# Performance work log

Measured on AMD Instinct MI355X. Metric: run time of the kernel, lower is better.

## Reference

```python
import jax, jax.numpy as jnp
import numpy as np

B, T, I, H, O = 128, 1024, 1, 512, 1


def setup_inputs() -> dict:
    key = jax.random.key(0)
    k = jax.random.split(key, 6)
    s = 1.0 / np.sqrt(H).astype(np.float32)
    x = jax.random.normal(k[0], (B, T, I), dtype=jnp.float32)
    Wx = jax.random.uniform(k[1], (I, 4 * H), jnp.float32, -s, s)   # input->gates
    Wh = jax.random.uniform(k[2], (H, 4 * H), jnp.float32, -s, s)   # hidden->gates
    b = jax.random.uniform(k[3], (4 * H,), jnp.float32, -s, s)      # gate bias
    Wl = jax.random.uniform(k[4], (H, O), jnp.float32, -s, s)       # readout
    bl = jax.random.uniform(k[5], (O,), jnp.float32, -s, s)
    return {"x": x, "Wx": Wx, "Wh": Wh, "b": b, "Wl": Wl, "bl": bl, "future": 0}


def reference(x, Wx, Wh, b, Wl, bl, future):
    # x: (B, T, I). Custom LSTM cell unrolled over time via lax.scan, with a
    # per-timestep linear readout (as in the original per-step loop).
    H_ = Wh.shape[0]
    h0 = jnp.zeros((x.shape[0], H_), dtype=x.dtype)
    c0 = jnp.zeros((x.shape[0], H_), dtype=x.dtype)

    def step(carry, xt):  # xt: (B, I)
        h, c = carry
        gates = xt @ Wx + h @ Wh + b            # (B, 4H)
        i, f, g, o = jnp.split(gates, 4, axis=-1)
        i = jax.nn.sigmoid(i)
        f = jax.nn.sigmoid(f)
        g = jnp.tanh(g)
        o = jax.nn.sigmoid(o)
        c = f * c + i * g
        h = o * jnp.tanh(c)
        y = h @ Wl + bl                          # (B, O)
        return (h, c), y

    (_, _), ys = jax.lax.scan(step, (h0, c0), jnp.swapaxes(x, 0, 1))
    # ys: (T, B, O) -> (B, T, O), matching torch.stack(outputs,1).squeeze(2)
    return jnp.swapaxes(ys, 0, 1)
```

## Files before the change

kernel.cpp:

```cpp
#include <hip/hip_runtime.h>
#include <hip/hip_fp16.h>


typedef _Float16 f16;
typedef _Float16 f16x8 __attribute__((ext_vector_type(8)));
typedef float f32x4 __attribute__((ext_vector_type(4)));

#define BATCH 128
#define TT 1024
#define HID 512

#define WPACK_OFF   0
#define WPACK_BYTES (16*4*2*16*64*16)
#define HBUF_OFF    WPACK_BYTES
#define HBUF_ELEMS  (BATCH*HID)
#define WL16_OFF    (HBUF_OFF + 4*HBUF_ELEMS*2)
#define HHIST_OFF   (WL16_OFF + 4096)
#define HHIST_BYTES ((size_t)TT * BATCH * HID * 2)
#define WS_NEEDED   ((size_t)HHIST_OFF + HHIST_BYTES)

__global__ __launch_bounds__(256) void init_kernel(const float* Wl, f16* wl16,
                                                   unsigned* hbuf) {
    int idx = blockIdx.x * 256 + threadIdx.x;
    hbuf[idx] = ((idx >> 15) == 0) ? 0u : 0x00010001u;
    if (idx < HID) wl16[idx] = (f16)Wl[idx];
}

__global__ __launch_bounds__(256) void pack_kernel(const float* __restrict__ Wh,
                                                   f16* __restrict__ wpack) {
    int tid  = blockIdx.x * 256 + threadIdx.x;
    int lane = tid & 63;
    int s    = (tid >> 6) & 15;
    int T    = (tid >> 10) & 1;
    int wv   = (tid >> 11) & 3;
    int cg   = tid >> 13;
    int l_lo = lane & 15, l_hi = lane >> 4;
    int jt = ((wv * 4) + s) & 15;
    int jj = l_lo >> 2, q = l_lo & 3;
    int c = q * 512 + cg * 32 + T * 16 + wv * 4 + jj;
    int kbase = jt * 32 + l_hi * 8;
    f16x8 v;
#pragma unroll
    for (int e = 0; e < 8; ++e) v[e] = (f16)Wh[(kbase + e) * 2048 + c];
    ((f16x8*)wpack)[tid] = v;
}

__device__ __forceinline__ float dot8(f16x8 a, f16x8 b, float acc) {
#if __has_builtin(__builtin_amdgcn_fdot2)
    acc = __builtin_amdgcn_fdot2(__builtin_shufflevector(a, a, 0, 1),
                                 __builtin_shufflevector(b, b, 0, 1), acc, false);
    acc = __builtin_amdgcn_fdot2(__builtin_shufflevector(a, a, 2, 3),
                                 __builtin_shufflevector(b, b, 2, 3), acc, false);
    acc = __builtin_amdgcn_fdot2(__builtin_shufflevector(a, a, 4, 5),
                                 __builtin_shufflevector(b, b, 4, 5), acc, false);
    acc = __builtin_amdgcn_fdot2(__builtin_shufflevector(a, a, 6, 7),
                                 __builtin_shufflevector(b, b, 6, 7), acc, false);
#else
#pragma unroll
    for (int e = 0; e < 8; ++e) acc += (float)a[e] * (float)b[e];
#endif
    return acc;
}

template<int CTRL>
__device__ __forceinline__ float dpp_qp(float v) {
    int r = __builtin_amdgcn_update_dpp(0, __builtin_bit_cast(int, v),
                                        CTRL, 0xF, 0xF, true);
    return __builtin_bit_cast(float, r);
}

__device__ __forceinline__ void quad_transpose(const f32x4& m, int p4,
                                               float& f0, float& f1,
                                               float& f2, float& f3) {
    float t0, e0, e1, e2, e3;
    t0 = dpp_qp<0xB1>(m[1]); e0 = (p4 & 1) ? t0 : m[0];
    t0 = dpp_qp<0xB1>(m[0]); e1 = (p4 & 1) ? m[1] : t0;
    t0 = dpp_qp<0xB1>(m[3]); e2 = (p4 & 1) ? t0 : m[2];
    t0 = dpp_qp<0xB1>(m[2]); e3 = (p4 & 1) ? m[3] : t0;
    t0 = dpp_qp<0x4E>(e2); f0 = (p4 & 2) ? t0 : e0;
    t0 = dpp_qp<0x4E>(e3); f1 = (p4 & 2) ? t0 : e1;
    t0 = dpp_qp<0x4E>(e0); f2 = (p4 & 2) ? e2 : t0;
    t0 = dpp_qp<0x4E>(e1); f3 = (p4 & 2) ? e3 : t0;
}

template<int MODE>
__global__ __launch_bounds__(256, 1) void lstm_kernel(
    const float* __restrict__ x, const float* __restrict__ Wx,
    const float* __restrict__ bvec, const float* __restrict__ blp,
    const f16* __restrict__ wpack, f16* __restrict__ hbuf,
    const f16* __restrict__ wl16, f16* __restrict__ hhist,
    float* __restrict__ out)
{
    const int tid = threadIdx.x;
    const int cg = blockIdx.x >> 3;
    const int bg = blockIdx.x & 7;
    const int w = tid >> 6, lane = tid & 63;
    const int l_lo = lane & 15, l_hi = lane >> 4;

    __shared__ f16 hsh[2][8192];
    __shared__ f16 wlsh[512];

    if (tid < 64)
        *(f16x8*)(wlsh + tid * 8) = *(const f16x8*)(wl16 + tid * 8);

    f16x8 bf0[16], bf1[16];
    {
        const f16x8* wp0 = (const f16x8*)wpack
                         + (size_t)(((cg * 4 + w) * 2 + 0) * 16) * 64 + lane;
        const f16x8* wp1 = (const f16x8*)wpack
                         + (size_t)(((cg * 4 + w) * 2 + 1) * 16) * 64 + lane;
#pragma unroll
        for (int s = 0; s < 16; ++s) { bf0[s] = wp0[s * 64]; bf1[s] = wp1[s * 64]; }
    }

    const int row  = l_hi * 4 + (l_lo & 3);
    const int u0 = cg * 32 + w * 4 + (l_lo >> 2);
    const int u1 = u0 + 16;
    const int bglob = bg * 16 + row;
    const float bi0 = bvec[0*512+u0], bfo0 = bvec[1*512+u0];
    const float bg0 = bvec[2*512+u0], bo0 = bvec[3*512+u0];
    const float bi1 = bvec[0*512+u1], bfo1 = bvec[1*512+u1];
    const float bg1 = bvec[2*512+u1], bo1 = bvec[3*512+u1];
    const float wxi0 = Wx[0*512+u0], wxf0 = Wx[1*512+u0];
    const float wxg0 = Wx[2*512+u0], wxo0 = Wx[3*512+u0];
    const float wxi1 = Wx[0*512+u1], wxf1 = Wx[1*512+u1];
    const float wxg1 = Wx[2*512+u1], wxo1 = Wx[3*512+u1];
    const float blv = blp[0];

    const int rd_base = bg * 8192 + ((w * 16 + l_hi) * 16 + l_lo) * 8;
    const int st_idx0 = bg * 8192 + ((u0 >> 3) * 16 + row) * 8 + (u0 & 7);
    const int st_idx1 = bg * 8192 + ((u1 >> 3) * 16 + row) * 8 + (u1 & 7);
    const int hist0 = (bg * 16 + row) * 512 + u0;
    const int hist1 = (bg * 16 + row) * 512 + u1;

    const int p4 = l_lo & 3;
    const int sx = (l_lo & 7) << 4;
    const int lbase = l_lo * 1024;
    const int base_ws = w * 256 + l_hi * 16;
    const int xrow = bglob * TT;

    float cst0 = 0.f, cst1 = 0.f;
    const int TLAST = (MODE == 0) ? (TT - 1) : TT;

    for (int t = 0; t <= TLAST; ++t) {
        const f16* hp = hbuf + (size_t)(t & 3) * HBUF_ELEMS + rd_base;
        const unsigned ep = (unsigned)((t >> 2) & 1) * 0x00010001u;
        float xv = x[xrow + (t < TT ? t : 0)];

        f16x8 s0, s1, s2, s3;
        for (;;) {
            asm volatile(
                "global_load_dwordx4 %0, %4, off sc0 sc1\n\t"
                "global_load_dwordx4 %1, %5, off sc0 sc1\n\t"
                "global_load_dwordx4 %2, %6, off sc0 sc1\n\t"
                "global_load_dwordx4 %3, %7, off sc0 sc1\n\t"
                "s_waitcnt vmcnt(0)"
                : "=&v"(s0), "=&v"(s1), "=&v"(s2), "=&v"(s3)
                : "v"(hp), "v"(hp + 512), "v"(hp + 1024), "v"(hp + 1536)
                : "memory");
            union { f16x8 v; unsigned u[4]; } b0, b1, b2, b3;
            b0.v = s0; b1.v = s1; b2.v = s2; b3.v = s3;
            unsigned bad =
                (((b0.u[0]^ep)|(b0.u[1]^ep)|(b0.u[2]^ep)|(b0.u[3]^ep)) |
                 ((b1.u[0]^ep)|(b1.u[1]^ep)|(b1.u[2]^ep)|(b1.u[3]^ep)) |
                 ((b2.u[0]^ep)|(b2.u[1]^ep)|(b2.u[2]^ep)|(b2.u[3]^ep)) |
                 ((b3.u[0]^ep)|(b3.u[1]^ep)|(b3.u[2]^ep)|(b3.u[3]^ep))) & 0x00010001u;
            if (__all(bad == 0u)) break;
        }
        __builtin_amdgcn_sched_barrier(0);

        char* hb = (char*)hsh[t & 1];
        const int wb = lbase + base_ws;
        *(f16x8*)(hb + ((wb +   0) ^ sx)) = s0;
        *(f16x8*)(hb + ((wb +  64) ^ sx)) = s1;
        *(f16x8*)(hb + ((wb + 128) ^ sx)) = s2;
        *(f16x8*)(hb + ((wb + 192) ^ sx)) = s3;

        f32x4 cA0 = {0,0,0,0}, cA1 = {0,0,0,0};
        if (t < TT) {
            cA0 = __builtin_amdgcn_mfma_f32_16x16x32_f16(s0, bf0[0], cA0, 0,0,0);
            cA1 = __builtin_amdgcn_mfma_f32_16x16x32_f16(s0, bf1[0], cA1, 0,0,0);
            cA0 = __builtin_amdgcn_mfma_f32_16x16x32_f16(s1, bf0[1], cA0, 0,0,0);
            cA1 = __builtin_amdgcn_mfma_f32_16x16x32_f16(s1, bf1[1], cA1, 0,0,0);
            cA0 = __builtin_amdgcn_mfma_f32_16x16x32_f16(s2, bf0[2], cA0, 0,0,0);
            cA1 = __builtin_amdgcn_mfma_f32_16x16x32_f16(s2, bf1[2], cA1, 0,0,0);
            cA0 = __builtin_amdgcn_mfma_f32_16x16x32_f16(s3, bf0[3], cA0, 0,0,0);
            cA1 = __builtin_amdgcn_mfma_f32_16x16x32_f16(s3, bf1[3], cA1, 0,0,0);
        }
        __syncthreads();

        if (t < TT) {
            f32x4 cB0 = {0,0,0,0}, cB1 = {0,0,0,0};
            f32x4 cC0 = {0,0,0,0}, cC1 = {0,0,0,0};
            f32x4 cD0 = {0,0,0,0}, cD1 = {0,0,0,0};
#pragma unroll
            for (int i = 0; i < 4; ++i) {
                f16x8 a1 = *(const f16x8*)(hb + ((lbase + ((base_ws + (4+i)*64) & 1023)) ^ sx));
                f16x8 a2 = *(const f16x8*)(hb + ((lbase + ((base_ws + (8+i)*64) & 1023)) ^ sx));
                f16x8 a3 = *(const f16x8*)(hb + ((lbase + ((base_ws + (12+i)*64) & 1023)) ^ sx));
                cB0 = __builtin_amdgcn_mfma_f32_16x16x32_f16(a1, bf0[ 4+i], cB0, 0,0,0);
                cB1 = __builtin_amdgcn_mfma_f32_16x16x32_f16(a1, bf1[ 4+i], cB1, 0,0,0);
                cC0 = __builtin_amdgcn_mfma_f32_16x16x32_f16(a2, bf0[ 8+i], cC0, 0,0,0);
                cC1 = __builtin_amdgcn_mfma_f32_16x16x32_f16(a2, bf1[ 8+i], cC1, 0,0,0);
                cD0 = __builtin_amdgcn_mfma_f32_16x16x32_f16(a3, bf0[12+i], cD0, 0,0,0);
                cD1 = __builtin_amdgcn_mfma_f32_16x16x32_f16(a3, bf1[12+i], cD1, 0,0,0);
            }
            f32x4 m0 = (cA0 + cB0) + (cC0 + cD0);
            f32x4 m1 = (cA1 + cB1) + (cC1 + cD1);

            float gi0, gf0, gg0, go0, gi1, gf1, gg1, go1;
            quad_transpose(m0, p4, gi0, gf0, gg0, go0);
            quad_transpose(m1, p4, gi1, gf1, gg1, go1);

            gi0 += xv * wxi0 + bi0;  gf0 += xv * wxf0 + bfo0;
            gg0 += xv * wxg0 + bg0;  go0 += xv * wxo0 + bo0;
            gi1 += xv * wxi1 + bi1;  gf1 += xv * wxf1 + bfo1;
            gg1 += xv * wxg1 + bg1;  go1 += xv * wxo1 + bo1;

            float iv0 = 1.f / (1.f + __expf(-gi0));
            float fv0 = 1.f / (1.f + __expf(-gf0));
            float gv0 = 2.f / (1.f + __expf(-2.f * gg0)) - 1.f;
            float ov0 = 1.f / (1.f + __expf(-go0));
            float iv1 = 1.f / (1.f + __expf(-gi1));
            float fv1 = 1.f / (1.f + __expf(-gf1));
            float gv1 = 2.f / (1.f + __expf(-2.f * gg1)) - 1.f;
            float ov1 = 1.f / (1.f + __expf(-go1));
            cst0 = fv0 * cst0 + iv0 * gv0;
            cst1 = fv1 * cst1 + iv1 * gv1;
            float hv0 = ov0 * (2.f / (1.f + __expf(-2.f * cst0)) - 1.f);
            float hv1 = ov1 * (2.f / (1.f + __expf(-2.f * cst1)) - 1.f);

            unsigned h0, h1;
            { union { f16 f; unsigned short s; } cv;
              cv.f = (f16)hv0; h0 = cv.s; cv.f = (f16)hv1; h1 = cv.s; }

            if ((MODE == 0) ? (t < TT - 1) : true) {
                const unsigned wtag = (unsigned)(((t + 1) >> 2) & 1);
                unsigned tg0 = (h0 & 0xFFFEu) | wtag;
                unsigned tg1 = (h1 & 0xFFFEu) | wtag;
                f16* dstb = hbuf + (size_t)((t + 1) & 3) * HBUF_ELEMS;
                asm volatile("global_store_short %0, %1, off sc0 sc1"
                             :: "v"(dstb + st_idx0), "v"(tg0) : "memory");
                asm volatile("global_store_short %0, %1, off sc0 sc1"
                             :: "v"(dstb + st_idx1), "v"(tg1) : "memory");
            }

            if (MODE == 0) {
                f16* hd = hhist + (size_t)t * (BATCH * HID);
                asm volatile("global_store_short %0, %1, off"
                             :: "v"(hd + hist0), "v"(h0) : "memory");
                asm volatile("global_store_short %0, %1, off"
                             :: "v"(hd + hist1), "v"(h1) : "memory");
            }
        }

        if (MODE == 1 && t >= 1 && cg == ((t >> 2) & 15) && w == (t & 3)) {
            float r0 = 0.f, r1 = 0.f, r2 = 0.f, r3 = 0.f;
#define WL(s) (*(const f16x8*)(wlsh + (((base_ws + (s)*64) & 1023) >> 1)))
            r0 = dot8(s0, WL(0), r0);
            r1 = dot8(s1, WL(1), r1);
            r2 = dot8(s2, WL(2), r2);
            r3 = dot8(s3, WL(3), r3);
#pragma unroll
            for (int i = 0; i < 4; ++i) {
                f16x8 a1 = *(const f16x8*)(hb + ((lbase + ((base_ws + (4+i)*64) & 1023)) ^ sx));
                f16x8 a2 = *(const f16x8*)(hb + ((lbase + ((base_ws + (8+i)*64) & 1023)) ^ sx));
                f16x8 a3 = *(const f16x8*)(hb + ((lbase + ((base_ws + (12+i)*64) & 1023)) ^ sx));
                r0 = dot8(a1, WL(4+i),  r0);
                r1 = dot8(a2, WL(8+i),  r1);
                r2 = dot8(a3, WL(12+i), r2);
            }
#undef WL
            float ry = (r0 + r1) + (r2 + r3);
            ry += __shfl_xor(ry, 16);
            ry += __shfl_xor(ry, 32);
            if (lane < 16)
                out[(bg * 16 + l_lo) * TT + (t - 1)] = blv + ry;
        }
    }
}

__global__ __launch_bounds__(256) void readout_kernel(
    const f16* __restrict__ hhist, const float* __restrict__ Wl,
    const float* __restrict__ blp, float* __restrict__ out)
{
    int gw = (blockIdx.x * 256 + threadIdx.x) >> 6;
    int lane = threadIdx.x & 63;
    int b = gw >> 7;
    int t0 = (gw & 127) * 8;
    const float4* wp = (const float4*)(Wl + lane * 8);
    float4 wa = wp[0], wb = wp[1];
    float blv = blp[0];
    const f16* hp = hhist + (size_t)t0 * (BATCH * HID) + b * HID + lane * 8;
#pragma unroll
    for (int j = 0; j < 8; ++j) {
        f16x8 h8 = *(const f16x8*)(hp + (size_t)j * (BATCH * HID));
        float p = (float)h8[0]*wa.x + (float)h8[1]*wa.y + (float)h8[2]*wa.z +
                  (float)h8[3]*wa.w + (float)h8[4]*wb.x + (float)h8[5]*wb.y +
                  (float)h8[6]*wb.z + (float)h8[7]*wb.w;
        p += __shfl_xor(p, 1);  p += __shfl_xor(p, 2);  p += __shfl_xor(p, 4);
        p += __shfl_xor(p, 8);  p += __shfl_xor(p, 16); p += __shfl_xor(p, 32);
        if (lane == 0) out[b * TT + t0 + j] = p + blv;
    }
}

extern "C" void kernel_launch(void* const* d_in, const int* in_sizes, int n_in,
                              void* d_out, int out_size, void* d_ws, size_t ws_size,
                              hipStream_t stream) {
    const float* x  = (const float*)d_in[0];
    const float* Wx = (const float*)d_in[1];
    const float* Wh = (const float*)d_in[2];
    const float* bv = (const float*)d_in[3];
    const float* Wl = (const float*)d_in[4];
    const float* bl = (const float*)d_in[5];
    float* out = (float*)d_out;
    char* ws = (char*)d_ws;

    f16* wpack = (f16*)(ws + WPACK_OFF);
    f16* hbuf  = (f16*)(ws + HBUF_OFF);
    f16* wl16  = (f16*)(ws + WL16_OFF);
    f16* hhist = (f16*)(ws + HHIST_OFF);

    init_kernel<<<512, 256, 0, stream>>>(Wl, wl16, (unsigned*)hbuf);
    pack_kernel<<<512, 256, 0, stream>>>(Wh, wpack);
    if (ws_size >= WS_NEEDED) {
        lstm_kernel<0><<<128, 256, 0, stream>>>(x, Wx, bv, bl, wpack, hbuf,
                                                wl16, hhist, out);
        readout_kernel<<<4096, 256, 0, stream>>>(hhist, Wl, bl, out);
    } else {
        lstm_kernel<1><<<128, 256, 0, stream>>>(x, Wx, bv, bl, wpack, hbuf,
                                                wl16, hhist, out);
    }
}
```

Baseline: 1.850 ms.

## Add shadow hidden-state buffer polled with sc0-only loads, periodic sc1 fallback

Each step's hidden state is now written to a second shadow buffer with device-scope (sc0) stores in addition to the system-coherent (sc0 sc1) buffer. The spin-wait poll reads the shadow copy with cheaper sc0 loads and falls back to the fully coherent buffer every eighth retry. The goal is to cut the latency of the inter-block exchange on the serial recurrence critical path. The cost is twice the store traffic per step, plus a risk of stale reads if sc0 loads do not observe cross-XCD writes, which the periodic sc1 fallback and tag check are meant to cover.

```diff
diff --git a/kernel.cpp b/kernel.cpp
--- a/kernel.cpp
+++ b/kernel.cpp
@@ -14,15 +14,18 @@
 #define WPACK_BYTES (16*4*2*16*64*16)
 #define HBUF_OFF    WPACK_BYTES
 #define HBUF_ELEMS  (BATCH*HID)
-#define WL16_OFF    (HBUF_OFF + 4*HBUF_ELEMS*2)
+#define SHBUF_OFF   (HBUF_OFF + 4*HBUF_ELEMS*2)
+#define WL16_OFF    (SHBUF_OFF + 4*HBUF_ELEMS*2)
 #define HHIST_OFF   (WL16_OFF + 4096)
 #define HHIST_BYTES ((size_t)TT * BATCH * HID * 2)
 #define WS_NEEDED   ((size_t)HHIST_OFF + HHIST_BYTES)
 
 __global__ __launch_bounds__(256) void init_kernel(const float* Wl, f16* wl16,
-                                                   unsigned* hbuf) {
+                                                   unsigned* hbuf, unsigned* hsh) {
     int idx = blockIdx.x * 256 + threadIdx.x;
-    hbuf[idx] = ((idx >> 15) == 0) ? 0u : 0x00010001u;
+    unsigned v = ((idx >> 15) == 0) ? 0u : 0x00010001u;
+    hbuf[idx] = v;
+    hsh[idx]  = v;
     if (idx < HID) wl16[idx] = (f16)Wl[idx];
 }
 
@@ -88,8 +91,8 @@
     const float* __restrict__ x, const float* __restrict__ Wx,
     const float* __restrict__ bvec, const float* __restrict__ blp,
     const f16* __restrict__ wpack, f16* __restrict__ hbuf,
-    const f16* __restrict__ wl16, f16* __restrict__ hhist,
-    float* __restrict__ out)
+    f16* __restrict__ hshadow, const f16* __restrict__ wl16,
+    f16* __restrict__ hhist, float* __restrict__ out)
 {
     const int tid = threadIdx.x;
     const int cg = blockIdx.x >> 3;
@@ -143,21 +146,35 @@
     const int TLAST = (MODE == 0) ? (TT - 1) : TT;
 
     for (int t = 0; t <= TLAST; ++t) {
-        const f16* hp = hbuf + (size_t)(t & 3) * HBUF_ELEMS + rd_base;
+        const f16* hp  = hbuf    + (size_t)(t & 3) * HBUF_ELEMS + rd_base;
+        const f16* hpS = hshadow + (size_t)(t & 3) * HBUF_ELEMS + rd_base;
         const unsigned ep = (unsigned)((t >> 2) & 1) * 0x00010001u;
         float xv = x[xrow + (t < TT ? t : 0)];
 
         f16x8 s0, s1, s2, s3;
+        unsigned r = 0;
         for (;;) {
-            asm volatile(
-                "global_load_dwordx4 %0, %4, off sc0 sc1\n\t"
-                "global_load_dwordx4 %1, %5, off sc0 sc1\n\t"
-                "global_load_dwordx4 %2, %6, off sc0 sc1\n\t"
-                "global_load_dwordx4 %3, %7, off sc0 sc1\n\t"
-                "s_waitcnt vmcnt(0)"
-                : "=&v"(s0), "=&v"(s1), "=&v"(s2), "=&v"(s3)
-                : "v"(hp), "v"(hp + 512), "v"(hp + 1024), "v"(hp + 1536)
-                : "memory");
+            if ((r++ & 7) != 7) {
+                asm volatile(
+                    "global_load_dwordx4 %0, %4, off sc0\n\t"
+                    "global_load_dwordx4 %1, %5, off sc0\n\t"
+                    "global_load_dwordx4 %2, %6, off sc0\n\t"
+                    "global_load_dwordx4 %3, %7, off sc0\n\t"
+                    "s_waitcnt vmcnt(0)"
+                    : "=&v"(s0), "=&v"(s1), "=&v"(s2), "=&v"(s3)
+                    : "v"(hpS), "v"(hpS + 512), "v"(hpS + 1024), "v"(hpS + 1536)
+                    : "memory");
+            } else {
+                asm volatile(
+                    "global_load_dwordx4 %0, %4, off sc0 sc1\n\t"
+                    "global_load_dwordx4 %1, %5, off sc0 sc1\n\t"
+                    "global_load_dwordx4 %2, %6, off sc0 sc1\n\t"
+                    "global_load_dwordx4 %3, %7, off sc0 sc1\n\t"
+                    "s_waitcnt vmcnt(0)"
+                    : "=&v"(s0), "=&v"(s1), "=&v"(s2), "=&v"(s3)
+                    : "v"(hp), "v"(hp + 512), "v"(hp + 1024), "v"(hp + 1536)
+                    : "memory");
+            }
             union { f16x8 v; unsigned u[4]; } b0, b1, b2, b3;
             b0.v = s0; b1.v = s1; b2.v = s2; b3.v = s3;
             unsigned bad =
@@ -238,7 +255,13 @@
                 const unsigned wtag = (unsigned)(((t + 1) >> 2) & 1);
                 unsigned tg0 = (h0 & 0xFFFEu) | wtag;
                 unsigned tg1 = (h1 & 0xFFFEu) | wtag;
-                f16* dstb = hbuf + (size_t)((t + 1) & 3) * HBUF_ELEMS;
+                size_t boff = (size_t)((t + 1) & 3) * HBUF_ELEMS;
+                f16* dstb = hbuf + boff;
+                f16* dstS = hshadow + boff;
+                asm volatile("global_store_short %0, %1, off sc0"
+                             :: "v"(dstS + st_idx0), "v"(tg0) : "memory");
+                asm volatile("global_store_short %0, %1, off sc0"
+                             :: "v"(dstS + st_idx1), "v"(tg1) : "memory");
                 asm volatile("global_store_short %0, %1, off sc0 sc1"
                              :: "v"(dstb + st_idx0), "v"(tg0) : "memory");
                 asm volatile("global_store_short %0, %1, off sc0 sc1"
@@ -316,19 +339,21 @@
     float* out = (float*)d_out;
     char* ws = (char*)d_ws;
 
-    f16* wpack = (f16*)(ws + WPACK_OFF);
-    f16* hbuf  = (f16*)(ws + HBUF_OFF);
-    f16* wl16  = (f16*)(ws + WL16_OFF);
-    f16* hhist = (f16*)(ws + HHIST_OFF);
-
-    init_kernel<<<512, 256, 0, stream>>>(Wl, wl16, (unsigned*)hbuf);
+    f16* wpack   = (f16*)(ws + WPACK_OFF);
+    f16* hbuf    = (f16*)(ws + HBUF_OFF);
+    f16* hshadow = (f16*)(ws + SHBUF_OFF);
+    f16* wl16    = (f16*)(ws + WL16_OFF);
+    f16* hhist   = (f16*)(ws + HHIST_OFF);
+
+    init_kernel<<<512, 256, 0, stream>>>(Wl, wl16, (unsigned*)hbuf,
+                                         (unsigned*)hshadow);
     pack_kernel<<<512, 256, 0, stream>>>(Wh, wpack);
     if (ws_size >= WS_NEEDED) {
         lstm_kernel<0><<<128, 256, 0, stream>>>(x, Wx, bv, bl, wpack, hbuf,
-                                                wl16, hhist, out);
+                                                hshadow, wl16, hhist, out);
         readout_kernel<<<4096, 256, 0, stream>>>(hhist, Wl, bl, out);
     } else {
         lstm_kernel<1><<<128, 256, 0, stream>>>(x, Wx, bv, bl, wpack, hbuf,
-                                                wl16, hhist, out);
+                                                hshadow, wl16, hhist, out);
     }
 }
```

Result: slower. 2.414 ms (+30.5%).

## Remap hidden units per lane and pack h stores into dwordx4 via shuffles

Applied to the files above, without the earlier changes.

Reassigns which hidden units each lane computes and permutes the K order of packed Wh and Wl so that each wave owns 8 contiguous hidden units. Each lane's two f16 h values are gathered across lanes with xor shuffles, so four lanes write 16-byte stores instead of every lane issuing scattered 2-byte stores. This applies to both the cross-block h exchange buffer and the history buffer. It aims to cut store instruction count and latency on the serial recurrence path, at the cost of extra shuffles and a permuted layout that the readout and consumers must match.

```diff
diff --git a/kernel.cpp b/kernel.cpp
--- a/kernel.cpp
+++ b/kernel.cpp
@@ -15,15 +15,25 @@
 #define HBUF_OFF    WPACK_BYTES
 #define HBUF_ELEMS  (BATCH*HID)
 #define WL16_OFF    (HBUF_OFF + 4*HBUF_ELEMS*2)
+#define WLP_OFF     (WL16_OFF + 1024)
 #define HHIST_OFF   (WL16_OFF + 4096)
 #define HHIST_BYTES ((size_t)TT * BATCH * HID * 2)
 #define WS_NEEDED   ((size_t)HHIST_OFF + HHIST_BYTES)
 
+__device__ __host__ __forceinline__ int kperm(int e) {
+    return (e >> 1) | ((e & 1) << 2);
+}
+
 __global__ __launch_bounds__(256) void init_kernel(const float* Wl, f16* wl16,
-                                                   unsigned* hbuf) {
+                                                   float* wlp, unsigned* hbuf) {
     int idx = blockIdx.x * 256 + threadIdx.x;
     hbuf[idx] = ((idx >> 15) == 0) ? 0u : 0x00010001u;
-    if (idx < HID) wl16[idx] = (f16)Wl[idx];
+    if (idx < HID) {
+        int kb = idx >> 3, e = idx & 7;
+        float v = Wl[kb * 8 + kperm(e)];
+        wl16[idx] = (f16)v;
+        wlp[idx] = v;
+    }
 }
 
 __global__ __launch_bounds__(256) void pack_kernel(const float* __restrict__ Wh,
@@ -37,11 +47,11 @@
     int l_lo = lane & 15, l_hi = lane >> 4;
     int jt = ((wv * 4) + s) & 15;
     int jj = l_lo >> 2, q = l_lo & 3;
-    int c = q * 512 + cg * 32 + T * 16 + wv * 4 + jj;
+    int c = q * 512 + cg * 32 + wv * 8 + T * 4 + jj;
     int kbase = jt * 32 + l_hi * 8;
     f16x8 v;
 #pragma unroll
-    for (int e = 0; e < 8; ++e) v[e] = (f16)Wh[(kbase + e) * 2048 + c];
+    for (int e = 0; e < 8; ++e) v[e] = (f16)Wh[(kbase + kperm(e)) * 2048 + c];
     ((f16x8*)wpack)[tid] = v;
 }
 
@@ -114,8 +124,8 @@
     }
 
     const int row  = l_hi * 4 + (l_lo & 3);
-    const int u0 = cg * 32 + w * 4 + (l_lo >> 2);
-    const int u1 = u0 + 16;
+    const int u0 = cg * 32 + w * 8 + (l_lo >> 2);
+    const int u1 = u0 + 4;
     const int bglob = bg * 16 + row;
     const float bi0 = bvec[0*512+u0], bfo0 = bvec[1*512+u0];
     const float bg0 = bvec[2*512+u0], bo0 = bvec[3*512+u0];
@@ -128,10 +138,9 @@
     const float blv = blp[0];
 
     const int rd_base = bg * 8192 + ((w * 16 + l_hi) * 16 + l_lo) * 8;
-    const int st_idx0 = bg * 8192 + ((u0 >> 3) * 16 + row) * 8 + (u0 & 7);
-    const int st_idx1 = bg * 8192 + ((u1 >> 3) * 16 + row) * 8 + (u1 & 7);
-    const int hist0 = (bg * 16 + row) * 512 + u0;
-    const int hist1 = (bg * 16 + row) * 512 + u1;
+    const int wrow = l_hi * 4 + l_lo;
+    const int st_base = bg * 8192 + (cg * 4 + w) * 128 + wrow * 8;
+    const size_t hist_base = (size_t)(bg * 16 + wrow) * HID + (cg * 4 + w) * 8;
 
     const int p4 = l_lo & 3;
     const int sx = (l_lo & 7) << 4;
@@ -234,23 +243,25 @@
             { union { f16 f; unsigned short s; } cv;
               cv.f = (f16)hv0; h0 = cv.s; cv.f = (f16)hv1; h1 = cv.s; }
 
-            if ((MODE == 0) ? (t < TT - 1) : true) {
-                const unsigned wtag = (unsigned)(((t + 1) >> 2) & 1);
-                unsigned tg0 = (h0 & 0xFFFEu) | wtag;
-                unsigned tg1 = (h1 & 0xFFFEu) | wtag;
-                f16* dstb = hbuf + (size_t)((t + 1) & 3) * HBUF_ELEMS;
-                asm volatile("global_store_short %0, %1, off sc0 sc1"
-                             :: "v"(dstb + st_idx0), "v"(tg0) : "memory");
-                asm volatile("global_store_short %0, %1, off sc0 sc1"
-                             :: "v"(dstb + st_idx1), "v"(tg1) : "memory");
-            }
-
-            if (MODE == 0) {
-                f16* hd = hhist + (size_t)t * (BATCH * HID);
-                asm volatile("global_store_short %0, %1, off"
-                             :: "v"(hd + hist0), "v"(h0) : "memory");
-                asm volatile("global_store_short %0, %1, off"
-                             :: "v"(hd + hist1), "v"(h1) : "memory");
+            const unsigned wtag = (unsigned)(((t + 1) >> 2) & 1);
+            unsigned p = ((h0 & 0xFFFEu) | wtag) | ((((h1 & 0xFFFEu) | wtag)) << 16);
+            unsigned q1 = (unsigned)__shfl_xor((int)p, 4);
+            unsigned q2 = (unsigned)__shfl_xor((int)p, 8);
+            unsigned q3 = (unsigned)__shfl_xor((int)q1, 8);
+            union { unsigned u[4]; f16x8 v; } pk;
+            pk.u[0] = p; pk.u[1] = q1; pk.u[2] = q2; pk.u[3] = q3;
+
+            if (l_lo < 4) {
+                if ((MODE == 0) ? (t < TT - 1) : true) {
+                    f16* dst = hbuf + (size_t)((t + 1) & 3) * HBUF_ELEMS + st_base;
+                    asm volatile("global_store_dwordx4 %0, %1, off sc0 sc1"
+                                 :: "v"(dst), "v"(pk.v) : "memory");
+                }
+                if (MODE == 0) {
+                    f16* hd = hhist + (size_t)t * (BATCH * HID) + hist_base;
+                    asm volatile("global_store_dwordx4 %0, %1, off"
+                                 :: "v"(hd), "v"(pk.v) : "memory");
+                }
             }
         }
 
@@ -281,14 +292,14 @@
 }
 
 __global__ __launch_bounds__(256) void readout_kernel(
-    const f16* __restrict__ hhist, const float* __restrict__ Wl,
+    const f16* __restrict__ hhist, const float* __restrict__ wlp,
     const float* __restrict__ blp, float* __restrict__ out)
 {
     int gw = (blockIdx.x * 256 + threadIdx.x) >> 6;
     int lane = threadIdx.x & 63;
     int b = gw >> 7;
     int t0 = (gw & 127) * 8;
-    const float4* wp = (const float4*)(Wl + lane * 8);
+    const float4* wp = (const float4*)(wlp + lane * 8);
     float4 wa = wp[0], wb = wp[1];
     float blv = blp[0];
     const f16* hp = hhist + (size_t)t0 * (BATCH * HID) + b * HID + lane * 8;
@@ -316,17 +327,18 @@
     float* out = (float*)d_out;
     char* ws = (char*)d_ws;
 
-    f16* wpack = (f16*)(ws + WPACK_OFF);
-    f16* hbuf  = (f16*)(ws + HBUF_OFF);
-    f16* wl16  = (f16*)(ws + WL16_OFF);
-    f16* hhist = (f16*)(ws + HHIST_OFF);
-
-    init_kernel<<<512, 256, 0, stream>>>(Wl, wl16, (unsigned*)hbuf);
+    f16* wpack  = (f16*)(ws + WPACK_OFF);
+    f16* hbuf   = (f16*)(ws + HBUF_OFF);
+    f16* wl16   = (f16*)(ws + WL16_OFF);
+    float* wlp  = (float*)(ws + WLP_OFF);
+    f16* hhist  = (f16*)(ws + HHIST_OFF);
+
+    init_kernel<<<512, 256, 0, stream>>>(Wl, wl16, wlp, (unsigned*)hbuf);
     pack_kernel<<<512, 256, 0, stream>>>(Wh, wpack);
     if (ws_size >= WS_NEEDED) {
         lstm_kernel<0><<<128, 256, 0, stream>>>(x, Wx, bv, bl, wpack, hbuf,
                                                 wl16, hhist, out);
-        readout_kernel<<<4096, 256, 0, stream>>>(hhist, Wl, bl, out);
+        readout_kernel<<<4096, 256, 0, stream>>>(hhist, wlp, bl, out);
     } else {
         lstm_kernel<1><<<128, 256, 0, stream>>>(x, Wx, bv, bl, wpack, hbuf,
                                                 wl16, hhist, out);
```

Measured after the change: 1.793 ms, median of 2. 3.1% less time.
